# Kernel tuning notes

Measured on AMD Instinct MI355X. Metric: run time of the kernel, lower is better.

Reference implementation:

```python
import jax, jax.numpy as jnp
import numpy as np

EPS_LN = 1e-6
EPS_NORM = 1e-12


def _l2_normalize(x):
    # F.normalize(p=2, dim=-1): x / max(||x||, eps)
    n = jnp.sqrt(jnp.sum(x * x, axis=-1, keepdims=True))
    return x / jnp.maximum(n, EPS_NORM)


def _layer_norm(x, g, b):
    mu = jnp.mean(x, axis=-1, keepdims=True)
    var = jnp.mean((x - mu) ** 2, axis=-1, keepdims=True)
    return (x - mu) / jnp.sqrt(var + EPS_LN) * g + b


def setup_inputs() -> dict:
    key = jax.random.key(0)
    ks = jax.random.split(key, 4)
    B, S1, S2, H = 16, 2048, 2048, 512
    return {
        "text1_output": jax.random.normal(ks[0], (B, S1, H), dtype=jnp.float32),
        "text2_output": jax.random.normal(ks[1], (B, S2, H), dtype=jnp.float32),
        "text1_mask": jnp.ones((B, S1), dtype=jnp.int32),
        "text2_mask": jnp.ones((B, S2), dtype=jnp.int32),
        "W1": jax.random.normal(ks[2], (H, 2 * H), dtype=jnp.float32) * (1.0 / np.sqrt(H)),
        "b1": jnp.zeros((2 * H,), dtype=jnp.float32),
        "W2": jax.random.normal(ks[3], (2 * H, H), dtype=jnp.float32) * (1.0 / np.sqrt(2 * H)),
        "b2": jnp.zeros((H,), dtype=jnp.float32),
        "ln1_g": jnp.ones((H,), dtype=jnp.float32),
        "ln1_b": jnp.zeros((H,), dtype=jnp.float32),
        "ln2_g": jnp.ones((H,), dtype=jnp.float32),
        "ln2_b": jnp.zeros((H,), dtype=jnp.float32),
    }


def reference(text1_output, text2_output, text1_mask, text2_mask,
              W1, b1, W2, b2, ln1_g, ln1_b, ln2_g, ln2_b):
    # Cosine-similarity cross-attention (dropout = identity, eval mode)
    q_norm = _l2_normalize(text1_output)            # [B,S1,H]
    k_norm = _l2_normalize(text2_output)            # [B,S2,H]
    sim = jnp.einsum('bsh,bth->bst', q_norm, k_norm)  # [B,S1,S2]
    sim = jnp.where(text2_mask[:, None, :] == 0, -jnp.inf, sim)
    attn = jax.nn.softmax(sim, axis=-1)
    out = jnp.einsum('bst,bth->bsh', attn, text2_output)  # [B,S1,H]

    norm_attn = _layer_norm(out, ln1_g, ln1_b)
    resid = norm_attn + text1_output

    ff = jnp.maximum(norm_attn @ W1 + b1, 0.0) @ W2 + b2
    norm_ff = _layer_norm(ff, ln2_g, ln2_b)
    return norm_ff + resid
```

## Files before the change

### kernel.cpp

```cpp
#include <hip/hip_runtime.h>
#include <stdint.h>

#define B_ 16
#define S1_ 2048
#define S2_ 2048
#define H_ 512

typedef short short8 __attribute__((ext_vector_type(8)));
typedef float f32x4 __attribute__((ext_vector_type(4)));
typedef long long2v __attribute__((ext_vector_type(2)));

__device__ __forceinline__ unsigned short f2bf(float f) {
  unsigned u = __builtin_bit_cast(unsigned, f);
  u += 0x7fffu + ((u >> 16) & 1u);
  return (unsigned short)(u >> 16);
}
__device__ __forceinline__ float bf2f(unsigned short us) {
  return __builtin_bit_cast(float, (unsigned)us << 16);
}

__device__ __forceinline__ void gload_lds16(const void* g, void* l) {
  __builtin_amdgcn_global_load_lds((const __attribute__((address_space(1))) void*)g,
                                   (__attribute__((address_space(3))) void*)l,
                                   16, 0, 0);
}

template <int WB16>
__global__ __launch_bounds__(256) void k_cast(const float* __restrict__ x,
                                              unsigned short* __restrict__ y,
                                              unsigned char* __restrict__ y8) {
  int row = blockIdx.x * 4 + (threadIdx.x >> 6);
  int l = threadIdx.x & 63;
  const f32x4* xr = (const f32x4*)(x + (size_t)row * H_) + l * 2;
  f32x4 a = xr[0], b = xr[1];
  float s = a[0]*a[0] + a[1]*a[1] + a[2]*a[2] + a[3]*a[3]
          + b[0]*b[0] + b[1]*b[1] + b[2]*b[2] + b[3]*b[3];
#pragma unroll
  for (int m = 1; m < 64; m <<= 1) s += __shfl_xor(s, m);
  float sc = 1.0f / fmaxf(sqrtf(s), 1e-12f);
  if (WB16) {
    short8 o;
#pragma unroll
    for (int i = 0; i < 4; ++i) { o[i] = (short)f2bf(a[i]); o[4 + i] = (short)f2bf(b[i]); }
    *(short8*)(y + (size_t)row * H_ + l * 8) = o;
  }
  int p0 = __builtin_amdgcn_cvt_pk_fp8_f32(a[0] * sc, a[1] * sc, 0, false);
  p0 = __builtin_amdgcn_cvt_pk_fp8_f32(a[2] * sc, a[3] * sc, p0, true);
  int p1 = __builtin_amdgcn_cvt_pk_fp8_f32(b[0] * sc, b[1] * sc, 0, false);
  p1 = __builtin_amdgcn_cvt_pk_fp8_f32(b[2] * sc, b[3] * sc, p1, true);
  int2 pk = {p0, p1};
  int poff = ((l >> 4) * 128) + ((l & 3) * 32) + (((l >> 2) & 3) * 8);
  *(int2*)(y8 + (size_t)row * H_ + poff) = pk;
}

__global__ __launch_bounds__(256) void k_tw(const float* __restrict__ Wm,
                                            unsigned short* __restrict__ WT,
                                            int lgR, int C) {
  int i = blockIdx.x * 256 + threadIdx.x;
  int R = 1 << lgR;
  int n = i >> lgR, k = i & (R - 1);
  WT[i] = f2bf(Wm[(size_t)k * C + n]);
}

__global__ __launch_bounds__(256) void k_tvt(const unsigned short* __restrict__ kn,
                                             unsigned short* __restrict__ vt) {
  __shared__ unsigned short tile[64][72];
  int h0 = blockIdx.x * 64, s0 = blockIdx.y * 64, b = blockIdx.z;
  int t = threadIdx.x;
#pragma unroll
  for (int p = 0; p < 2; ++p) {
    int si = p * 32 + (t >> 3);
    int cj = (t & 7) * 8;
    short8 v = *(const short8*)(kn + ((size_t)(b * S2_ + s0 + si)) * H_ + h0 + cj);
#pragma unroll
    for (int x = 0; x < 8; ++x) tile[si][cj + x] = (unsigned short)v[x];
  }
  __syncthreads();
#pragma unroll
  for (int p = 0; p < 2; ++p) {
    int ho = p * 32 + (t >> 3);
    int sx = (t & 7) * 8;
    short8 o;
#pragma unroll
    for (int x = 0; x < 8; ++x) o[x] = (short)tile[sx + x][ho];
    *(short8*)(vt + ((size_t)(b * H_ + h0 + ho)) * S2_ + s0 + sx) = o;
  }
}

template <int MODE, int SWZ, int FP8>
__global__ __launch_bounds__(256, 2) void k_gemm(
    const void* __restrict__ A, const void* __restrict__ BT,
    const float* __restrict__ bias, const int* __restrict__ mask,
    void* __restrict__ out,
    int M, int N, int K, long sAbytes, long sBbytes, long sOut) {
  __shared__ char lA[16384];
  __shared__ char lB[16384];

  int bx, by, z;
  if (SWZ) {
    const int gx = gridDim.x, gy = gridDim.y;
    const int nwg = gx * gy * (int)gridDim.z;
    int orig = ((int)blockIdx.z * gy + (int)blockIdx.y) * gx + (int)blockIdx.x;
    int swzid = ((nwg & 7) == 0) ? ((orig & 7) * (nwg >> 3) + (orig >> 3)) : orig;
    z = swzid / (gx * gy);
    int rem = swzid - z * (gx * gy);
    by = rem / gx;
    bx = rem - by * gx;
  } else {
    bx = blockIdx.x; by = blockIdx.y; z = blockIdx.z;
  }

  const int w = threadIdx.x >> 6, l = threadIdx.x & 63;
  const int lr = l & 15, lk = l >> 4;
  const int m0 = by * 128, n0 = bx * 128;
  const int wm = (w >> 1) * 64, wn = (w & 1) * 64;

  const size_t rowbytes = (size_t)K * (FP8 ? 1 : 2);
  const int srow = l >> 3;
  const int lswz = ((l & 7) * 16) ^ ((srow & 7) << 4);
  const char* pA = (const char*)A + (size_t)z * sAbytes + (size_t)(m0 + w * 8 + srow) * rowbytes + lswz;
  const char* pB = (const char*)BT + (size_t)z * sBbytes + (size_t)(n0 + w * 8 + srow) * rowbytes + lswz;
  const size_t rstep = rowbytes * 32;

  f32x4 acc[4][4];
#pragma unroll
  for (int i = 0; i < 4; ++i)
#pragma unroll
    for (int j = 0; j < 4; ++j) acc[i][j] = (f32x4){0.f, 0.f, 0.f, 0.f};

  const int NT = K >> (FP8 ? 7 : 6);

#pragma unroll 1
  for (int t = 0; t < NT; ++t) {
    const size_t kb = (size_t)t * 128;
#pragma unroll
    for (int j = 0; j < 4; ++j) {
      gload_lds16(pA + j * rstep + kb, lA + (j * 4 + w) * 1024);
      gload_lds16(pB + j * rstep + kb, lB + (j * 4 + w) * 1024);
    }
    asm volatile("s_waitcnt vmcnt(0)" ::: "memory");
    __syncthreads();
    if (FP8) {
#pragma unroll
      for (int s2 = 0; s2 < 2; ++s2) {
        long2v af[4], bf[4];
#pragma unroll
        for (int mi = 0; mi < 4; ++mi) {
          int row = wm + mi * 16 + lr;
          short8 tmp = *(const short8*)(lA + row * 128 + ((lk * 32 + s2 * 16) ^ ((row & 7) << 4)));
          af[mi] = __builtin_bit_cast(long2v, tmp);
        }
#pragma unroll
        for (int ni = 0; ni < 4; ++ni) {
          int row = wn + ni * 16 + lr;
          short8 tmp = *(const short8*)(lB + row * 128 + ((lk * 32 + s2 * 16) ^ ((row & 7) << 4)));
          bf[ni] = __builtin_bit_cast(long2v, tmp);
        }
#pragma unroll
        for (int mi = 0; mi < 4; ++mi)
#pragma unroll
          for (int ni = 0; ni < 4; ++ni) {
            acc[mi][ni] = __builtin_amdgcn_mfma_f32_16x16x32_fp8_fp8(af[mi].x, bf[ni].x, acc[mi][ni], 0, 0, 0);
            acc[mi][ni] = __builtin_amdgcn_mfma_f32_16x16x32_fp8_fp8(af[mi].y, bf[ni].y, acc[mi][ni], 0, 0, 0);
          }
      }
    } else {
      const unsigned short* As = (const unsigned short*)lA;
      const unsigned short* Bs = (const unsigned short*)lB;
#pragma unroll
      for (int s = 0; s < 2; ++s) {
        short8 af[4], bf[4];
#pragma unroll
        for (int mi = 0; mi < 4; ++mi) {
          int row = wm + mi * 16 + lr;
          af[mi] = *(const short8*)(As + row * 64 + ((s * 32 + lk * 8) ^ ((row & 7) << 3)));
        }
#pragma unroll
        for (int ni = 0; ni < 4; ++ni) {
          int row = wn + ni * 16 + lr;
          bf[ni] = *(const short8*)(Bs + row * 64 + ((s * 32 + lk * 8) ^ ((row & 7) << 3)));
        }
#pragma unroll
        for (int mi = 0; mi < 4; ++mi)
#pragma unroll
          for (int ni = 0; ni < 4; ++ni)
            acc[mi][ni] = __builtin_amdgcn_mfma_f32_16x16x32_bf16(af[mi], bf[ni], acc[mi][ni], 0, 0, 0);
      }
    }
    __syncthreads();
  }

  if (MODE == 2) {
    float mv[4];
#pragma unroll
    for (int ni = 0; ni < 4; ++ni) {
      int gn = n0 + wn + ni * 16 + lr;
      mv[ni] = (mask[(size_t)z * N + gn] != 0) ? 1.0f : 0.0f;
    }
#pragma unroll
    for (int mi = 0; mi < 4; ++mi)
#pragma unroll
      for (int ni = 0; ni < 4; ++ni) {
        int gn = n0 + wn + ni * 16 + lr;
#pragma unroll
        for (int r = 0; r < 4; ++r) {
          int gm = m0 + wm + mi * 16 + lk * 4 + r;
          float p = __expf(acc[mi][ni][r] - 1.0f) * mv[ni];
          ((unsigned short*)out)[(size_t)z * sOut + (size_t)gm * N + gn] = f2bf(p);
        }
      }
  } else if (MODE == 3) {
#pragma unroll
    for (int mi = 0; mi < 4; ++mi)
#pragma unroll
      for (int r = 0; r < 4; ++r) {
        int gm = m0 + wm + mi * 16 + lk * 4 + r;
#pragma unroll
        for (int ni = 0; ni < 4; ++ni) {
          int gn = n0 + wn + ni * 16 + lr;
          ((unsigned short*)out)[(size_t)z * sOut + (size_t)gm * N + gn] = f2bf(acc[mi][ni][r]);
        }
      }
  } else {
#pragma unroll
    for (int mi = 0; mi < 4; ++mi)
#pragma unroll
      for (int ni = 0; ni < 4; ++ni) {
        int gn = n0 + wn + ni * 16 + lr;
        float bs = bias[gn];
#pragma unroll
        for (int r = 0; r < 4; ++r) {
          int gm = m0 + wm + mi * 16 + lk * 4 + r;
          float v = acc[mi][ni][r] + bs;
          if (MODE == 0) v = fmaxf(v, 0.f);
          ((unsigned short*)out)[(size_t)gm * N + gn] = f2bf(v);
        }
      }
  }
}

__global__ __launch_bounds__(256) void k_ln1(const unsigned short* __restrict__ O,
                                             const float* __restrict__ g,
                                             const float* __restrict__ bvec,
                                             unsigned short* __restrict__ nattn) {
  int row = blockIdx.x * 4 + (threadIdx.x >> 6);
  int l = threadIdx.x & 63;
  size_t base = (size_t)row * H_ + l * 8;
  short8 ov = *(const short8*)(O + base);
  float x[8];
#pragma unroll
  for (int i = 0; i < 8; ++i) x[i] = bf2f((unsigned short)ov[i]);
  float s = 0.f, q = 0.f;
#pragma unroll
  for (int i = 0; i < 8; ++i) { s += x[i]; q += x[i] * x[i]; }
#pragma unroll
  for (int m = 1; m < 64; m <<= 1) { s += __shfl_xor(s, m); q += __shfl_xor(q, m); }
  float mean = s * (1.f / 512.f);
  float var = q * (1.f / 512.f) - mean * mean;
  float rstd = rsqrtf(var + 1e-6f);
  f32x4 g0 = *(const f32x4*)(g + l * 8), g1v = *(const f32x4*)(g + l * 8 + 4);
  f32x4 b0 = *(const f32x4*)(bvec + l * 8), b1v = *(const f32x4*)(bvec + l * 8 + 4);
  short8 no;
#pragma unroll
  for (int i = 0; i < 4; ++i) {
    no[i]     = (short)f2bf((x[i] - mean) * rstd * g0[i] + b0[i]);
    no[4 + i] = (short)f2bf((x[4 + i] - mean) * rstd * g1v[i] + b1v[i]);
  }
  *(short8*)(nattn + base) = no;
}

__global__ __launch_bounds__(256) void k_ln2(const unsigned short* __restrict__ ff,
                                             const unsigned short* __restrict__ nattn,
                                             const float* __restrict__ text1,
                                             const float* __restrict__ g2,
                                             const float* __restrict__ bb2,
                                             float* __restrict__ out) {
  int row = blockIdx.x * 4 + (threadIdx.x >> 6);
  int l = threadIdx.x & 63;
  size_t base = (size_t)row * H_ + l * 8;
  short8 fv = *(const short8*)(ff + base);
  float x[8];
#pragma unroll
  for (int i = 0; i < 8; ++i) x[i] = bf2f((unsigned short)fv[i]);
  float s = 0.f, q = 0.f;
#pragma unroll
  for (int i = 0; i < 8; ++i) { s += x[i]; q += x[i] * x[i]; }
#pragma unroll
  for (int m = 1; m < 64; m <<= 1) { s += __shfl_xor(s, m); q += __shfl_xor(q, m); }
  float mean = s * (1.f / 512.f);
  float var = q * (1.f / 512.f) - mean * mean;
  float rstd = rsqrtf(var + 1e-6f);
  f32x4 g0 = *(const f32x4*)(g2 + l * 8), g1v = *(const f32x4*)(g2 + l * 8 + 4);
  f32x4 b0 = *(const f32x4*)(bb2 + l * 8), b1v = *(const f32x4*)(bb2 + l * 8 + 4);
  short8 nv = *(const short8*)(nattn + base);
  f32x4 t0 = *(const f32x4*)(text1 + base), t1 = *(const f32x4*)(text1 + base + 4);
  f32x4 o0, o1;
#pragma unroll
  for (int i = 0; i < 4; ++i) {
    o0[i] = (x[i] - mean) * rstd * g0[i] + b0[i] + bf2f((unsigned short)nv[i]) + t0[i];
    o1[i] = (x[4 + i] - mean) * rstd * g1v[i] + b1v[i] + bf2f((unsigned short)nv[4 + i]) + t1[i];
  }
  *(f32x4*)(out + base) = o0;
  *(f32x4*)(out + base + 4) = o1;
}

extern "C" void kernel_launch(void* const* d_in, const int* in_sizes, int n_in,
                              void* d_out, int out_size, void* d_ws, size_t ws_size,
                              hipStream_t stream) {
  const float* text1 = (const float*)d_in[0];
  const float* text2 = (const float*)d_in[1];
  const int* mask2 = (const int*)d_in[3];
  const float* W1 = (const float*)d_in[4];
  const float* b1 = (const float*)d_in[5];
  const float* W2 = (const float*)d_in[6];
  const float* b2 = (const float*)d_in[7];
  const float* g1 = (const float*)d_in[8];
  const float* bb1 = (const float*)d_in[9];
  const float* g2 = (const float*)d_in[10];
  const float* bb2 = (const float*)d_in[11];

  const size_t MiB = 1024ull * 1024ull;
  char* ws = (char*)d_ws;
  unsigned short* W1T   = (unsigned short*)(ws + 0 * MiB);
  unsigned short* W2T   = (unsigned short*)(ws + 1 * MiB);
  unsigned char*  qn8   = (unsigned char*)(ws + 4 * MiB);
  unsigned char*  kn8   = (unsigned char*)(ws + 20 * MiB);
  unsigned short* kn    = (unsigned short*)(ws + 36 * MiB);
  unsigned short* vt    = (unsigned short*)(ws + 164 * MiB);
  unsigned short* P     = (unsigned short*)(ws + 36 * MiB);
  unsigned short* O     = (unsigned short*)(ws + 4 * MiB);
  unsigned short* nattn = (unsigned short*)(ws + 100 * MiB);
  unsigned short* hbuf  = (unsigned short*)(ws + 132 * MiB);
  unsigned short* ffb   = (unsigned short*)(ws + 36 * MiB);
  float* outp = (float*)d_out;

  k_cast<0><<<dim3(B_ * S1_ / 4), 256, 0, stream>>>(text1, nullptr, qn8);
  k_cast<1><<<dim3(B_ * S2_ / 4), 256, 0, stream>>>(text2, kn, kn8);
  k_tw<<<dim3(512 * 1024 / 256), 256, 0, stream>>>(W1, W1T, 9, 1024);
  k_tw<<<dim3(512 * 1024 / 256), 256, 0, stream>>>(W2, W2T, 10, 512);
  k_tvt<<<dim3(H_ / 64, S2_ / 64, B_), 256, 0, stream>>>(kn, vt);

  k_gemm<2, 0, 1><<<dim3(S2_ / 128, S1_ / 128, B_), 256, 0, stream>>>(
      qn8, kn8, nullptr, mask2,
      P, S1_, S2_, H_, (long)S1_ * H_, (long)S2_ * H_, (long)S1_ * S2_);
  k_gemm<3, 1, 0><<<dim3(H_ / 128, S1_ / 128, B_), 256, 0, stream>>>(
      P, vt, nullptr, nullptr,
      O, S1_, H_, S2_, (long)S1_ * S2_ * 2, (long)H_ * S2_ * 2, (long)S1_ * H_);

  k_ln1<<<dim3(B_ * S1_ / 4), 256, 0, stream>>>(O, g1, bb1, nattn);
  k_gemm<0, 1, 0><<<dim3(1024 / 128, 32768 / 128, 1), 256, 0, stream>>>(
      nattn, W1T, b1, nullptr, hbuf, 32768, 1024, 512, 0, 0, 0);
  k_gemm<1, 1, 0><<<dim3(512 / 128, 32768 / 128, 1), 256, 0, stream>>>(
      hbuf, W2T, b2, nullptr, ffb, 32768, 512, 1024, 0, 0, 0);
  k_ln2<<<dim3(32768 / 4), 256, 0, stream>>>(ffb, nattn, text1, g2, bb2, outp);
}
```

Before: 289.5 us.

## Double-buffer LDS tiles in GEMM to overlap global loads with MFMA

Splits the LDS A/B tiles into two buffers and prefetches the next K tile into the alternate buffer while the current one is consumed, waiting with a partial vmcnt so only the older loads must complete. Raw s_barrier calls replace __syncthreads. This is meant to hide global-to-LDS latency behind matrix math. The cost is doubled LDS (64KB per block), which may lower occupancy below the requested 2 blocks per CU.

```diff
diff --git a/kernel.cpp b/kernel.cpp
--- a/kernel.cpp
+++ b/kernel.cpp
@@ -93,8 +93,8 @@
     const float* __restrict__ bias, const int* __restrict__ mask,
     void* __restrict__ out,
     int M, int N, int K, long sAbytes, long sBbytes, long sOut) {
-  __shared__ char lA[16384];
-  __shared__ char lB[16384];
+  __shared__ char lA[2][16384];
+  __shared__ char lB[2][16384];
 
   int bx, by, z;
   if (SWZ) {
@@ -130,30 +130,45 @@
 
   const int NT = K >> (FP8 ? 7 : 6);
 
+#pragma unroll
+  for (int j = 0; j < 4; ++j) {
+    gload_lds16(pA + j * rstep, lA[0] + (j * 4 + w) * 1024);
+    gload_lds16(pB + j * rstep, lB[0] + (j * 4 + w) * 1024);
+  }
+
 #pragma unroll 1
   for (int t = 0; t < NT; ++t) {
-    const size_t kb = (size_t)t * 128;
-#pragma unroll
-    for (int j = 0; j < 4; ++j) {
-      gload_lds16(pA + j * rstep + kb, lA + (j * 4 + w) * 1024);
-      gload_lds16(pB + j * rstep + kb, lB + (j * 4 + w) * 1024);
+    const int cur = t & 1;
+    if (t + 1 < NT) {
+      const size_t kb = (size_t)(t + 1) * 128;
+#pragma unroll
+      for (int j = 0; j < 4; ++j) {
+        gload_lds16(pA + j * rstep + kb, lA[cur ^ 1] + (j * 4 + w) * 1024);
+        gload_lds16(pB + j * rstep + kb, lB[cur ^ 1] + (j * 4 + w) * 1024);
+      }
+      asm volatile("s_waitcnt vmcnt(8)" ::: "memory");
+    } else {
+      asm volatile("s_waitcnt vmcnt(0)" ::: "memory");
     }
-    asm volatile("s_waitcnt vmcnt(0)" ::: "memory");
-    __syncthreads();
+    __builtin_amdgcn_s_barrier();
+    asm volatile("" ::: "memory");
+
     if (FP8) {
+      const char* As = lA[cur];
+      const char* Bs = lB[cur];
 #pragma unroll
       for (int s2 = 0; s2 < 2; ++s2) {
         long2v af[4], bf[4];
 #pragma unroll
         for (int mi = 0; mi < 4; ++mi) {
           int row = wm + mi * 16 + lr;
-          short8 tmp = *(const short8*)(lA + row * 128 + ((lk * 32 + s2 * 16) ^ ((row & 7) << 4)));
+          short8 tmp = *(const short8*)(As + row * 128 + ((lk * 32 + s2 * 16) ^ ((row & 7) << 4)));
           af[mi] = __builtin_bit_cast(long2v, tmp);
         }
 #pragma unroll
         for (int ni = 0; ni < 4; ++ni) {
           int row = wn + ni * 16 + lr;
-          short8 tmp = *(const short8*)(lB + row * 128 + ((lk * 32 + s2 * 16) ^ ((row & 7) << 4)));
+          short8 tmp = *(const short8*)(Bs + row * 128 + ((lk * 32 + s2 * 16) ^ ((row & 7) << 4)));
           bf[ni] = __builtin_bit_cast(long2v, tmp);
         }
 #pragma unroll
@@ -165,8 +180,8 @@
           }
       }
     } else {
-      const unsigned short* As = (const unsigned short*)lA;
-      const unsigned short* Bs = (const unsigned short*)lB;
+      const unsigned short* As = (const unsigned short*)lA[cur];
+      const unsigned short* Bs = (const unsigned short*)lB[cur];
 #pragma unroll
       for (int s = 0; s < 2; ++s) {
         short8 af[4], bf[4];
@@ -187,7 +202,9 @@
             acc[mi][ni] = __builtin_amdgcn_mfma_f32_16x16x32_bf16(af[mi], bf[ni], acc[mi][ni], 0, 0, 0);
       }
     }
-    __syncthreads();
+
+    asm volatile("" ::: "memory");
+    __builtin_amdgcn_s_barrier();
   }
 
   if (MODE == 2) {
```

Result: slower. 335.8 us (+16.0%).
